# Performance work log

Hardware: AMD Instinct MI355X
Metric: run time of the kernel (lower is better)

The kernel has to match this reference:

```python
import jax, jax.numpy as jnp
import numpy as np

N = 50000   # nodes
E = 600000  # edges
D = 128     # in_channels == heads*hidden_channels
OUT = 64    # out_channels
L = 3       # local_layers
EPS = 1e-5  # BatchNorm eps


def setup_inputs() -> dict:
    key = jax.random.key(0)
    ks = jax.random.split(key, 10)
    s = 0.05
    x = jax.random.normal(ks[0], (N, D), jnp.float32)
    edge_index = jax.random.randint(ks[1], (2, E), 0, N, dtype=jnp.int32)
    Wg = jax.random.normal(ks[2], (L, D, D), jnp.float32) * s  # GCNConv weights
    bg = jnp.zeros((L, D), jnp.float32)                         # GCNConv biases
    Wl = jax.random.normal(ks[3], (L, D, D), jnp.float32) * s  # residual Linear weights
    bl = jax.random.normal(ks[4], (L, D), jnp.float32) * s
    gamma = jnp.ones((L, D), jnp.float32)                       # BN scale
    beta = jnp.zeros((L, D), jnp.float32)                       # BN shift
    Wp = jax.random.normal(ks[5], (D, OUT), jnp.float32) * s   # pred head
    bp = jnp.zeros((OUT,), jnp.float32)
    return {"x": x, "edge_index": edge_index, "Wg": Wg, "bg": bg,
            "Wl": Wl, "bl": bl, "gamma": gamma, "beta": beta,
            "Wp": Wp, "bp": bp}


def reference(x, edge_index, Wg, bg, Wl, bl, gamma, beta, Wp, bp):
    src, dst = edge_index[0], edge_index[1]
    # GCN symmetric normalization with self-loops (PyG gcn_norm):
    # deg computed on target (col) including self-loop.
    deg = jax.ops.segment_sum(jnp.ones((E,), x.dtype), dst, num_segments=N) + 1.0
    dinv = jax.lax.rsqrt(deg)                      # deg^{-1/2}, [N]
    enorm = dinv[src] * dinv[dst]                  # per-edge norm, [E]
    self_norm = (dinv * dinv)[:, None]             # deg^{-1} for self-loop, [N,1]

    h = x
    x_local = jnp.zeros((N, D), x.dtype)
    for i in range(L):
        hg = h @ Wg[i]                             # [N, D] transformed features
        # gather -> weight -> scatter-add (message passing) + self-loop term
        agg = jax.ops.segment_sum(hg[src] * enorm[:, None], dst, num_segments=N)
        conv = agg + hg * self_norm + bg[i]
        # residual linear
        h = conv + h @ Wl[i] + bl[i]
        # BatchNorm1d (training-mode batch statistics, biased var)
        mu = jnp.mean(h, axis=0)
        var = jnp.mean(jnp.square(h - mu), axis=0)
        h = (h - mu) * jax.lax.rsqrt(var + EPS) * gamma[i] + beta[i]
        h = jax.nn.relu(h)
        x_local = x_local + h                      # add_ accumulation
    return x_local @ Wp + bp
```

## Files before the change

### kernel.cpp

```cpp
#include <hip/hip_runtime.h>

#define D 128
#define OUTC 64
#define EC 256

typedef float floatx4 __attribute__((ext_vector_type(4)));
typedef short short8 __attribute__((ext_vector_type(8)));

__device__ inline unsigned short f2bf(float f) {
  unsigned int u = __float_as_uint(f);
  unsigned int r = (u + 0x7FFF + ((u >> 16) & 1)) >> 16;
  return (unsigned short)r;
}
__device__ inline float bf2f(unsigned short u) {
  return __uint_as_float(((unsigned int)u) << 16);
}

__device__ inline int swz(int row, int k) { return row * 128 + (k ^ ((row & 7) << 3)); }

__global__ __launch_bounds__(256) void k_prepx(const float* __restrict__ x, unsigned short* __restrict__ xb, int total4) {
  int stride = gridDim.x * blockDim.x;
  for (int i = blockIdx.x * blockDim.x + threadIdx.x; i < total4; i += stride) {
    float4 v = ((const float4*)x)[i];
    ushort4 o;
    o.x = f2bf(v.x); o.y = f2bf(v.y); o.z = f2bf(v.z); o.w = f2bf(v.w);
    ((ushort4*)xb)[i] = o;
  }
}

__global__ __launch_bounds__(256) void k_prepw(const float* __restrict__ Wg, const float* __restrict__ Wl,
                                               const float* __restrict__ Wp,
                                               unsigned short* __restrict__ Wgt, unsigned short* __restrict__ Wlt,
                                               unsigned short* __restrict__ Wpt) {
  int u = blockIdx.x * 256 + threadIdx.x;
  const int W1 = 3 * D * D;
  if (u < W1) {
    int i = u / (D * D), rem = u % (D * D);
    int k = rem / D, n = rem % D;
    Wgt[i * D * D + n * D + k] = f2bf(Wg[u]);
  } else if (u < 2 * W1) {
    int v = u - W1;
    int i = v / (D * D), rem = v % (D * D);
    int k = rem / D, n = rem % D;
    Wlt[i * D * D + n * D + k] = f2bf(Wl[v]);
  } else if (u < 2 * W1 + D * OUTC) {
    int v = u - 2 * W1;
    int k = v / OUTC, n = v % OUTC;
    Wpt[n * D + k] = f2bf(Wp[v]);
  }
}


__global__ __launch_bounds__(256) void k_bh(const int* __restrict__ dst, int* __restrict__ bh,
                                            int E, int nbuk, int chk) {
  __shared__ int hist[256];
  int t = threadIdx.x, c = blockIdx.x;
  hist[t] = 0;
  __syncthreads();
  int s = c * chk, e = min(E, s + chk);
  for (int j = s + t; j < e; j += 256)
    atomicAdd(&hist[dst[j] >> 8], 1);
  __syncthreads();
  if (t < nbuk) bh[t * EC + c] = hist[t];
}

__device__ inline int block_scan4(int4 v, int t, int* total) {
  int s = v.x + v.y + v.z + v.w;
  int lane = t & 63, w = t >> 6;
  int incl = s;
  #pragma unroll
  for (int off = 1; off < 64; off <<= 1) {
    int nb = __shfl_up(incl, off);
    if (lane >= off) incl += nb;
  }
  __shared__ int wsum[4];
  if (lane == 63) wsum[w] = incl;
  __syncthreads();
  int woff = 0;
  #pragma unroll
  for (int k = 0; k < 3; ++k) if (w > k) woff += wsum[k];
  if (total) *total = wsum[0] + wsum[1] + wsum[2] + wsum[3];
  return woff + incl - s;
}

__global__ __launch_bounds__(256) void k_gscan1(int* __restrict__ arr, int* __restrict__ bsum, int n) {
  int t = threadIdx.x;
  int i0 = blockIdx.x * 1024 + t * 4;
  int4 v = make_int4(0, 0, 0, 0);
  if (i0 + 3 < n) v = *(const int4*)(arr + i0);
  else {
    if (i0 < n) v.x = arr[i0];
    if (i0 + 1 < n) v.y = arr[i0 + 1];
    if (i0 + 2 < n) v.z = arr[i0 + 2];
    if (i0 + 3 < n) v.w = arr[i0 + 3];
  }
  int total;
  int e = block_scan4(v, t, &total);
  if (i0 < n) {
    int4 o;
    o.x = e; o.y = e + v.x; o.z = o.y + v.y; o.w = o.z + v.z;
    if (i0 + 3 < n) *(int4*)(arr + i0) = o;
    else {
      arr[i0] = o.x;
      if (i0 + 1 < n) arr[i0 + 1] = o.y;
      if (i0 + 2 < n) arr[i0 + 2] = o.z;
    }
  }
  if (t == 0) bsum[blockIdx.x] = total;
}

__global__ __launch_bounds__(256) void k_gscan2(int* __restrict__ bsum, int nb) {
  int t = threadIdx.x;
  int i0 = t * 4;
  int4 v = make_int4(0, 0, 0, 0);
  if (i0 + 3 < nb) v = *(const int4*)(bsum + i0);
  else {
    if (i0 < nb) v.x = bsum[i0];
    if (i0 + 1 < nb) v.y = bsum[i0 + 1];
    if (i0 + 2 < nb) v.z = bsum[i0 + 2];
    if (i0 + 3 < nb) v.w = bsum[i0 + 3];
  }
  int e = block_scan4(v, t, nullptr);
  if (i0 < nb) {
    bsum[i0] = e;
    if (i0 + 1 < nb) bsum[i0 + 1] = e + v.x;
    if (i0 + 2 < nb) bsum[i0 + 2] = e + v.x + v.y;
    if (i0 + 3 < nb) bsum[i0 + 3] = e + v.x + v.y + v.z;
  }
}

__global__ __launch_bounds__(256) void k_scatter(const int* __restrict__ src, const int* __restrict__ dst,
                                                 const int* __restrict__ bhs, const int* __restrict__ bsum,
                                                 unsigned int* __restrict__ ebuk, int E, int nbuk, int chk) {
  __shared__ int cur[256];
  int t = threadIdx.x, c = blockIdx.x;
  if (t < nbuk) {
    int idx = t * EC + c;
    cur[t] = bhs[idx] + bsum[idx >> 10];
  }
  __syncthreads();
  int s = c * chk, e = min(E, s + chk);
  for (int j = s + t; j < e; j += 256) {
    int d = dst[j];
    int pos = atomicAdd(&cur[d >> 8], 1);
    ebuk[pos] = (unsigned int)src[j] | ((unsigned int)(d & 255) << 24);
  }
}

__global__ __launch_bounds__(256) void k_csr(const unsigned int* __restrict__ ebuk, const int* __restrict__ bhs,
                                             const int* __restrict__ bsum,
                                             int* __restrict__ rowstart, int* __restrict__ csr,
                                             float* __restrict__ dinv, int E, int N, int nbuk) {
  __shared__ int cnt[256];
  __shared__ int wsum[4];
  int t = threadIdx.x, b = blockIdx.x;
  int si = b * EC;
  int s = bhs[si] + bsum[si >> 10];
  int e;
  if (b + 1 < nbuk) { int ei_ = (b + 1) * EC; e = bhs[ei_] + bsum[ei_ >> 10]; }
  else e = E;
  cnt[t] = 0;
  __syncthreads();
  for (int j = s + t; j < e; j += 256)
    atomicAdd(&cnt[ebuk[j] >> 24], 1);
  __syncthreads();
  int v = cnt[t];
  int lane = t & 63, w = t >> 6;
  int incl = v;
  #pragma unroll
  for (int off = 1; off < 64; off <<= 1) {
    int nb = __shfl_up(incl, off);
    if (lane >= off) incl += nb;
  }
  if (lane == 63) wsum[w] = incl;
  __syncthreads();
  int woff = 0;
  #pragma unroll
  for (int k = 0; k < 3; ++k) if (w > k) woff += wsum[k];
  int rs = s + woff + incl - v;
  int node = (b << 8) + t;
  __syncthreads();
  cnt[t] = rs;
  if (node < N) {
    rowstart[node] = rs;
    dinv[node] = rsqrtf((float)v + 1.0f);
  }
  if (node == 0) rowstart[N] = E;
  __syncthreads();
  for (int j = s + t; j < e; j += 256) {
    unsigned int ed = ebuk[j];
    int pos = atomicAdd(&cnt[ed >> 24], 1);
    csr[pos] = (int)(ed & 0xFFFFFFu);
  }
}

__global__ __launch_bounds__(256) void k_dual(const unsigned short* __restrict__ Ab,
                                              const unsigned short* __restrict__ Wgt,
                                              const unsigned short* __restrict__ Wlt,
                                              const float* __restrict__ bg, const float* __restrict__ bl,
                                              unsigned short* __restrict__ hg, unsigned short* __restrict__ hl, int M) {
  __shared__ unsigned short As[64 * 128];
  __shared__ unsigned short Bs[128 * 128];
  int tid = threadIdx.x;
  int row0 = blockIdx.x * 64;

  {
    int r = tid >> 2;
    int row = row0 + r;
    const unsigned short* src = Ab + (size_t)row * D;
    #pragma unroll
    for (int j = 0; j < 4; ++j) {
      int c = (tid & 3) + j * 4;
      short8 v = {0, 0, 0, 0, 0, 0, 0, 0};
      if (row < M) v = *(const short8*)(src + c * 8);
      *(short8*)&As[swz(r, c * 8)] = v;
    }
  }
  #pragma unroll
  for (int j = 0; j < 8; ++j) {
    int idx = tid + j * 256;
    int nr = idx >> 4, c = idx & 15;
    *(short8*)&Bs[swz(nr, c * 8)] = *(const short8*)(Wgt + nr * D + c * 8);
  }
  __syncthreads();

  int lane = tid & 63, w = tid >> 6;
  int lrow = lane & 15, lk = (lane >> 4) * 8;

  short8 af[4][4];
  #pragma unroll
  for (int m = 0; m < 4; ++m) {
    int ar = lrow + m * 16;
    #pragma unroll
    for (int kk = 0; kk < 4; ++kk)
      af[m][kk] = *(const short8*)&As[swz(ar, lk + kk * 32)];
  }

  {
    short8 bfg[2][4];
    #pragma unroll
    for (int n = 0; n < 2; ++n) {
      int br = w * 32 + n * 16 + lrow;
      #pragma unroll
      for (int kk = 0; kk < 4; ++kk)
        bfg[n][kk] = *(const short8*)&Bs[swz(br, lk + kk * 32)];
    }
    floatx4 acc[4][2];
    #pragma unroll
    for (int m = 0; m < 4; ++m)
      #pragma unroll
      for (int n = 0; n < 2; ++n)
        acc[m][n] = (floatx4)0.0f;
    #pragma unroll
    for (int kk = 0; kk < 4; ++kk)
      #pragma unroll
      for (int m = 0; m < 4; ++m)
        #pragma unroll
        for (int n = 0; n < 2; ++n)
          acc[m][n] = __builtin_amdgcn_mfma_f32_16x16x32_bf16(af[m][kk], bfg[n][kk], acc[m][n], 0, 0, 0);
    #pragma unroll
    for (int m = 0; m < 4; ++m)
      #pragma unroll
      for (int n = 0; n < 2; ++n) {
        int col = w * 32 + n * 16 + lrow;
        #pragma unroll
        for (int reg = 0; reg < 4; ++reg) {
          int row = row0 + m * 16 + (lane >> 4) * 4 + reg;
          if (row < M) hg[(size_t)row * D + col] = f2bf(acc[m][n][reg]);
        }
      }
  }
  __syncthreads();
  #pragma unroll
  for (int j = 0; j < 8; ++j) {
    int idx = tid + j * 256;
    int nr = idx >> 4, c = idx & 15;
    *(short8*)&Bs[swz(nr, c * 8)] = *(const short8*)(Wlt + nr * D + c * 8);
  }
  __syncthreads();
  {
    short8 bfl[2][4];
    #pragma unroll
    for (int n = 0; n < 2; ++n) {
      int br = w * 32 + n * 16 + lrow;
      #pragma unroll
      for (int kk = 0; kk < 4; ++kk)
        bfl[n][kk] = *(const short8*)&Bs[swz(br, lk + kk * 32)];
    }
    floatx4 acc[4][2];
    #pragma unroll
    for (int m = 0; m < 4; ++m)
      #pragma unroll
      for (int n = 0; n < 2; ++n)
        acc[m][n] = (floatx4)0.0f;
    #pragma unroll
    for (int kk = 0; kk < 4; ++kk)
      #pragma unroll
      for (int m = 0; m < 4; ++m)
        #pragma unroll
        for (int n = 0; n < 2; ++n)
          acc[m][n] = __builtin_amdgcn_mfma_f32_16x16x32_bf16(af[m][kk], bfl[n][kk], acc[m][n], 0, 0, 0);
    #pragma unroll
    for (int m = 0; m < 4; ++m)
      #pragma unroll
      for (int n = 0; n < 2; ++n) {
        int col = w * 32 + n * 16 + lrow;
        float bias = bg[col] + bl[col];
        #pragma unroll
        for (int reg = 0; reg < 4; ++reg) {
          int row = row0 + m * 16 + (lane >> 4) * 4 + reg;
          if (row < M) hl[(size_t)row * D + col] = f2bf(acc[m][n][reg] + bias);
        }
      }
  }
}

__global__ __launch_bounds__(256) void k_agg(const unsigned short* __restrict__ hg, unsigned short* __restrict__ pre,
                                             const int* __restrict__ rowstart, const int* __restrict__ csr,
                                             const float* __restrict__ dinv,
                                             float* __restrict__ partial, int n) {
  int t = threadIdx.x, b = blockIdx.x;
  int w = t >> 6, lane = t & 63;
  const unsigned int* base = (const unsigned int*)hg;
  unsigned int* prew = (unsigned int*)pre;
  float st_s0 = 0.f, st_s1 = 0.f, st_q0 = 0.f, st_q1 = 0.f;
  int c = lane * 2;
  int node0 = b * 16 + w * 4;
  #pragma unroll 1
  for (int k = 0; k < 4; ++k) {
    int node = node0 + k;
    if (node >= n) break;
    int s = rowstart[node], e = rowstart[node + 1];
    float dn = dinv[node];
    unsigned int ps = base[(size_t)node * 64 + lane];
    unsigned int oldw = prew[(size_t)node * 64 + lane];
    float a0 = 0.f, a1 = 0.f, b0 = 0.f, b1 = 0.f;
    float c0 = 0.f, c1 = 0.f, d0 = 0.f, d1 = 0.f;
    int j = s;
    for (; j + 4 <= e; j += 4) {
      int sn0 = csr[j], sn1 = csr[j + 1], sn2 = csr[j + 2], sn3 = csr[j + 3];
      float w0 = dinv[sn0], w1 = dinv[sn1], w2 = dinv[sn2], w3 = dinv[sn3];
      unsigned int p0 = base[(size_t)sn0 * 64 + lane];
      unsigned int p1 = base[(size_t)sn1 * 64 + lane];
      unsigned int p2 = base[(size_t)sn2 * 64 + lane];
      unsigned int p3 = base[(size_t)sn3 * 64 + lane];
      a0 += w0 * __uint_as_float(p0 << 16); a1 += w0 * __uint_as_float(p0 & 0xFFFF0000u);
      b0 += w1 * __uint_as_float(p1 << 16); b1 += w1 * __uint_as_float(p1 & 0xFFFF0000u);
      c0 += w2 * __uint_as_float(p2 << 16); c1 += w2 * __uint_as_float(p2 & 0xFFFF0000u);
      d0 += w3 * __uint_as_float(p3 << 16); d1 += w3 * __uint_as_float(p3 & 0xFFFF0000u);
    }
    for (; j < e; ++j) {
      int sn = csr[j];
      float wv = dinv[sn];
      unsigned int p = base[(size_t)sn * 64 + lane];
      a0 += wv * __uint_as_float(p << 16);
      a1 += wv * __uint_as_float(p & 0xFFFF0000u);
    }
    float acc0 = (a0 + b0) + (c0 + d0);
    float acc1 = (a1 + b1) + (c1 + d1);
    float sf = dn * dn;
    float h0 = __uint_as_float(ps << 16);
    float h1 = __uint_as_float(ps & 0xFFFF0000u);
    float old0 = __uint_as_float(oldw << 16);
    float old1 = __uint_as_float(oldw & 0xFFFF0000u);
    float p0 = dn * acc0 + h0 * sf + old0;
    float p1 = dn * acc1 + h1 * sf + old1;
    prew[(size_t)node * 64 + lane] = (unsigned int)f2bf(p0) | ((unsigned int)f2bf(p1) << 16);
    st_s0 += p0; st_s1 += p1;
    st_q0 += p0 * p0; st_q1 += p1 * p1;
  }
  __shared__ float sm[4][128], sq[4][128];
  sm[w][c] = st_s0; sm[w][c + 1] = st_s1;
  sq[w][c] = st_q0; sq[w][c + 1] = st_q1;
  __syncthreads();
  if (t < 128) {
    float s = (sm[0][t] + sm[1][t]) + (sm[2][t] + sm[3][t]);
    float q = (sq[0][t] + sq[1][t]) + (sq[2][t] + sq[3][t]);
    partial[(size_t)b * 256 + t] = s;
    partial[(size_t)b * 256 + 128 + t] = q;
  }
}

__global__ __launch_bounds__(256) void k_fina(const float* __restrict__ partial, float* __restrict__ p2, int nab) {
  int t = threadIdx.x, b = blockIdx.x;
  float s = 0.f;
  for (int i = b; i < nab; i += 64)
    s += partial[(size_t)i * 256 + t];
  p2[(size_t)b * 256 + t] = s;
}

__global__ __launch_bounds__(256) void k_finb(const float* __restrict__ p2,
                                              const float* __restrict__ gamma, const float* __restrict__ beta,
                                              float* __restrict__ ab, float invN) {
  int t = threadIdx.x;
  float s = 0.f;
  #pragma unroll
  for (int b = 0; b < 64; ++b)
    s += p2[(size_t)b * 256 + t];
  __shared__ float red[256];
  red[t] = s;
  __syncthreads();
  if (t < 128) {
    float mean = red[t] * invN;
    float var = red[128 + t] * invN - mean * mean;
    float inv = rsqrtf(var + 1e-5f);
    float g = gamma[t];
    ab[t] = g * inv;
    ab[128 + t] = beta[t] - mean * inv * g;
  }
}

template<bool FIRST>
__global__ __launch_bounds__(256) void k_fused(const unsigned short* __restrict__ pre, const float* __restrict__ ab,
                                               const unsigned short* __restrict__ Wpt, const float* __restrict__ bp,
                                               const unsigned short* __restrict__ Wgt,
                                               const unsigned short* __restrict__ Wlt,
                                               const float* __restrict__ bgn, const float* __restrict__ bln,
                                               float* __restrict__ out, unsigned short* __restrict__ hg,
                                               unsigned short* __restrict__ hl, int M) {
  __shared__ unsigned short As[64 * 128];
  __shared__ unsigned short Bs[128 * 128];
  int tid = threadIdx.x;
  int row0 = blockIdx.x * 64;

  {
    int r = tid >> 2, qq = tid & 3;
    int row = row0 + r;
    bool valid = row < M;
    const unsigned short* Pp = pre + (size_t)row * D;
    #pragma unroll
    for (int ch = 0; ch < 4; ++ch) {
      int k0 = qq * 32 + ch * 8;
      short8 pv = {0, 0, 0, 0, 0, 0, 0, 0};
      if (valid) pv = *(const short8*)(Pp + k0);
      float4 a0 = *(const float4*)(ab + k0),        a1 = *(const float4*)(ab + k0 + 4);
      float4 b0 = *(const float4*)(ab + 128 + k0),  b1 = *(const float4*)(ab + 128 + k0 + 4);
      float av[8] = {a0.x, a0.y, a0.z, a0.w, a1.x, a1.y, a1.z, a1.w};
      float bv[8] = {b0.x, b0.y, b0.z, b0.w, b1.x, b1.y, b1.z, b1.w};
      unsigned short hv[8];
      #pragma unroll
      for (int jj = 0; jj < 8; ++jj) {
        float f = bf2f((unsigned short)pv[jj]);
        hv[jj] = f2bf(fmaxf(f * av[jj] + bv[jj], 0.f));
      }
      *(short8*)&As[swz(r, k0)] = *(const short8*)hv;
    }
  }
  #pragma unroll
  for (int j = 0; j < 4; ++j) {
    int idx = tid + j * 256;
    int nr = idx >> 4, c = idx & 15;
    *(short8*)&Bs[swz(nr, c * 8)] = *(const short8*)(Wpt + nr * D + c * 8);
  }
  __syncthreads();

  int lane = tid & 63, w = tid >> 6;
  int lrow = lane & 15, lk = (lane >> 4) * 8;

  short8 af[4][4];
  #pragma unroll
  for (int m = 0; m < 4; ++m) {
    int ar = lrow + m * 16;
    #pragma unroll
    for (int kk = 0; kk < 4; ++kk)
      af[m][kk] = *(const short8*)&As[swz(ar, lk + kk * 32)];
  }

  {
    short8 bfr[4];
    int br = w * 16 + lrow;
    #pragma unroll
    for (int kk = 0; kk < 4; ++kk)
      bfr[kk] = *(const short8*)&Bs[swz(br, lk + kk * 32)];
    floatx4 acc[4];
    #pragma unroll
    for (int m = 0; m < 4; ++m) acc[m] = (floatx4)0.0f;
    #pragma unroll
    for (int kk = 0; kk < 4; ++kk)
      #pragma unroll
      for (int m = 0; m < 4; ++m)
        acc[m] = __builtin_amdgcn_mfma_f32_16x16x32_bf16(af[m][kk], bfr[kk], acc[m], 0, 0, 0);
    int col = w * 16 + lrow;
    float bpv = FIRST ? bp[col] : 0.f;
    #pragma unroll
    for (int m = 0; m < 4; ++m)
      #pragma unroll
      for (int reg = 0; reg < 4; ++reg) {
        int row = row0 + m * 16 + (lane >> 4) * 4 + reg;
        if (row < M) {
          float* op = &out[(size_t)row * OUTC + col];
          float v = acc[m][reg] + bpv;
          if (!FIRST) v += *op;
          *op = v;
        }
      }
  }
  __syncthreads();
  #pragma unroll
  for (int j = 0; j < 8; ++j) {
    int idx = tid + j * 256;
    int nr = idx >> 4, c = idx & 15;
    *(short8*)&Bs[swz(nr, c * 8)] = *(const short8*)(Wgt + nr * D + c * 8);
  }
  __syncthreads();
  {
    short8 bfg[2][4];
    #pragma unroll
    for (int n = 0; n < 2; ++n) {
      int br = w * 32 + n * 16 + lrow;
      #pragma unroll
      for (int kk = 0; kk < 4; ++kk)
        bfg[n][kk] = *(const short8*)&Bs[swz(br, lk + kk * 32)];
    }
    floatx4 acc[4][2];
    #pragma unroll
    for (int m = 0; m < 4; ++m)
      #pragma unroll
      for (int n = 0; n < 2; ++n)
        acc[m][n] = (floatx4)0.0f;
    #pragma unroll
    for (int kk = 0; kk < 4; ++kk)
      #pragma unroll
      for (int m = 0; m < 4; ++m)
        #pragma unroll
        for (int n = 0; n < 2; ++n)
          acc[m][n] = __builtin_amdgcn_mfma_f32_16x16x32_bf16(af[m][kk], bfg[n][kk], acc[m][n], 0, 0, 0);
    #pragma unroll
    for (int m = 0; m < 4; ++m)
      #pragma unroll
      for (int n = 0; n < 2; ++n) {
        int col = w * 32 + n * 16 + lrow;
        #pragma unroll
        for (int reg = 0; reg < 4; ++reg) {
          int row = row0 + m * 16 + (lane >> 4) * 4 + reg;
          if (row < M) hg[(size_t)row * D + col] = f2bf(acc[m][n][reg]);
        }
      }
  }
  __syncthreads();
  #pragma unroll
  for (int j = 0; j < 8; ++j) {
    int idx = tid + j * 256;
    int nr = idx >> 4, c = idx & 15;
    *(short8*)&Bs[swz(nr, c * 8)] = *(const short8*)(Wlt + nr * D + c * 8);
  }
  __syncthreads();
  {
    short8 bfl[2][4];
    #pragma unroll
    for (int n = 0; n < 2; ++n) {
      int br = w * 32 + n * 16 + lrow;
      #pragma unroll
      for (int kk = 0; kk < 4; ++kk)
        bfl[n][kk] = *(const short8*)&Bs[swz(br, lk + kk * 32)];
    }
    floatx4 acc[4][2];
    #pragma unroll
    for (int m = 0; m < 4; ++m)
      #pragma unroll
      for (int n = 0; n < 2; ++n)
        acc[m][n] = (floatx4)0.0f;
    #pragma unroll
    for (int kk = 0; kk < 4; ++kk)
      #pragma unroll
      for (int m = 0; m < 4; ++m)
        #pragma unroll
        for (int n = 0; n < 2; ++n)
          acc[m][n] = __builtin_amdgcn_mfma_f32_16x16x32_bf16(af[m][kk], bfl[n][kk], acc[m][n], 0, 0, 0);
    #pragma unroll
    for (int m = 0; m < 4; ++m)
      #pragma unroll
      for (int n = 0; n < 2; ++n) {
        int col = w * 32 + n * 16 + lrow;
        float bias = bgn[col] + bln[col];
        #pragma unroll
        for (int reg = 0; reg < 4; ++reg) {
          int row = row0 + m * 16 + (lane >> 4) * 4 + reg;
          if (row < M) hl[(size_t)row * D + col] = f2bf(acc[m][n][reg] + bias);
        }
      }
  }
}

__global__ __launch_bounds__(256) void k_out(const unsigned short* __restrict__ pre, const float* __restrict__ ab,
                                             const unsigned short* __restrict__ Wpt,
                                             float* __restrict__ out, int M) {
  __shared__ unsigned short As[64 * 128];
  __shared__ unsigned short Bs[OUTC * 128];
  int tid = threadIdx.x;
  int row0 = blockIdx.x * 64;

  {
    int r = tid >> 2, qq = tid & 3;
    int row = row0 + r;
    bool valid = row < M;
    const unsigned short* Pp = pre + (size_t)row * D;
    #pragma unroll
    for (int ch = 0; ch < 4; ++ch) {
      int k0 = qq * 32 + ch * 8;
      short8 pv = {0, 0, 0, 0, 0, 0, 0, 0};
      if (valid) pv = *(const short8*)(Pp + k0);
      float4 a0 = *(const float4*)(ab + k0),        a1 = *(const float4*)(ab + k0 + 4);
      float4 b0 = *(const float4*)(ab + 128 + k0),  b1 = *(const float4*)(ab + 128 + k0 + 4);
      float av[8] = {a0.x, a0.y, a0.z, a0.w, a1.x, a1.y, a1.z, a1.w};
      float bv[8] = {b0.x, b0.y, b0.z, b0.w, b1.x, b1.y, b1.z, b1.w};
      unsigned short hv[8];
      #pragma unroll
      for (int jj = 0; jj < 8; ++jj) {
        float f = bf2f((unsigned short)pv[jj]);
        hv[jj] = f2bf(fmaxf(f * av[jj] + bv[jj], 0.f));
      }
      *(short8*)&As[swz(r, k0)] = *(const short8*)hv;
    }
  }
  #pragma unroll
  for (int j = 0; j < 4; ++j) {
    int idx = tid + j * 256;
    int nr = idx >> 4, c = idx & 15;
    *(short8*)&Bs[swz(nr, c * 8)] = *(const short8*)(Wpt + nr * D + c * 8);
  }
  __syncthreads();

  int lane = tid & 63, w = tid >> 6;
  int lrow = lane & 15, lk = (lane >> 4) * 8;

  short8 af[4][4];
  #pragma unroll
  for (int m = 0; m < 4; ++m) {
    int ar = lrow + m * 16;
    #pragma unroll
    for (int kk = 0; kk < 4; ++kk)
      af[m][kk] = *(const short8*)&As[swz(ar, lk + kk * 32)];
  }
  short8 bfr[4];
  {
    int br = w * 16 + lrow;
    #pragma unroll
    for (int kk = 0; kk < 4; ++kk)
      bfr[kk] = *(const short8*)&Bs[swz(br, lk + kk * 32)];
  }
  floatx4 acc[4];
  #pragma unroll
  for (int m = 0; m < 4; ++m) acc[m] = (floatx4)0.0f;
  #pragma unroll
  for (int kk = 0; kk < 4; ++kk)
    #pragma unroll
    for (int m = 0; m < 4; ++m)
      acc[m] = __builtin_amdgcn_mfma_f32_16x16x32_bf16(af[m][kk], bfr[kk], acc[m], 0, 0, 0);

  int col = w * 16 + lrow;
  #pragma unroll
  for (int m = 0; m < 4; ++m)
    #pragma unroll
    for (int reg = 0; reg < 4; ++reg) {
      int row = row0 + m * 16 + (lane >> 4) * 4 + reg;
      if (row < M) {
        float* op = &out[(size_t)row * OUTC + col];
        *op = *op + acc[m][reg];
      }
    }
}

extern "C" void kernel_launch(void* const* d_in, const int* in_sizes, int n_in,
                              void* d_out, int out_size, void* d_ws, size_t ws_size,
                              hipStream_t stream) {
  const float* x     = (const float*)d_in[0];
  const int*   ei    = (const int*)d_in[1];
  const float* Wg    = (const float*)d_in[2];
  const float* bg    = (const float*)d_in[3];
  const float* Wl    = (const float*)d_in[4];
  const float* bl    = (const float*)d_in[5];
  const float* gamma = (const float*)d_in[6];
  const float* beta  = (const float*)d_in[7];
  const float* Wp    = (const float*)d_in[8];
  const float* bp    = (const float*)d_in[9];
  float* out = (float*)d_out;

  int N = in_sizes[0] / D;
  int E = in_sizes[1] / 2;
  const int* srcp = ei;
  const int* dstp = ei + E;

  char* wsb = (char*)d_ws;
  size_t off = 0;
  auto alloc = [&](size_t bytes) {
    off = (off + 255) & ~(size_t)255;
    void* p = wsb + off;
    off += bytes;
    return p;
  };
  int nab = (N + 15) / 16;
  float* dinv     = (float*)alloc((size_t)N * 4);
  int*   rowstart = (int*)alloc((size_t)(N + 1) * 4);
  int*   csr      = (int*)alloc((size_t)E * 4);
  int*   bh       = (int*)alloc((size_t)256 * EC * 4);
  unsigned int* ebuk = (unsigned int*)alloc((size_t)E * 4);
  int*   bsum     = (int*)alloc(1024 * 4);
  float* partial  = (float*)alloc((size_t)nab * 256 * 4);
  float* p2       = (float*)alloc((size_t)64 * 256 * 4);
  float* ab       = (float*)alloc(3 * 256 * 4);
  unsigned short* xb  = (unsigned short*)alloc((size_t)N * D * 2);
  unsigned short* hg  = (unsigned short*)alloc((size_t)N * D * 2);
  unsigned short* hl  = (unsigned short*)alloc((size_t)N * D * 2);
  unsigned short* Wgt = (unsigned short*)alloc(3 * D * D * 2);
  unsigned short* Wlt = (unsigned short*)alloc(3 * D * D * 2);
  unsigned short* Wpt = (unsigned short*)alloc(D * OUTC * 2);
  (void)ws_size; (void)n_in; (void)out_size;

  k_prepx<<<1024, 256, 0, stream>>>(x, xb, N * D / 4);
  int wtotal = 2 * 3 * D * D + D * OUTC;
  k_prepw<<<(wtotal + 255) / 256, 256, 0, stream>>>(Wg, Wl, Wp, Wgt, Wlt, Wpt);

  int nbuk = (N + 255) >> 8;
  int chk  = (E + EC - 1) / EC;
  k_bh<<<EC, 256, 0, stream>>>(dstp, bh, E, nbuk, chk);
  int sn  = nbuk * EC;
  int snb = (sn + 1023) >> 10;
  k_gscan1<<<snb, 256, 0, stream>>>(bh, bsum, sn);
  k_gscan2<<<1, 256, 0, stream>>>(bsum, snb);
  k_scatter<<<EC, 256, 0, stream>>>(srcp, dstp, bh, bsum, ebuk, E, nbuk, chk);
  k_csr<<<nbuk, 256, 0, stream>>>(ebuk, bh, bsum, rowstart, csr, dinv, E, N, nbuk);

  int mt = (N + 63) / 64;
  float invN = 1.0f / (float)N;

  k_dual<<<mt, 256, 0, stream>>>(xb, Wgt, Wlt, bg, bl, hg, hl, N);

  for (int i = 0; i < 3; ++i) {
    k_agg<<<nab, 256, 0, stream>>>(hg, hl, rowstart, csr, dinv, partial, N);
    k_fina<<<64, 256, 0, stream>>>(partial, p2, nab);
    k_finb<<<1, 256, 0, stream>>>(p2, gamma + (size_t)i * D, beta + (size_t)i * D, ab + i * 256, invN);
    if (i == 0)
      k_fused<true><<<mt, 256, 0, stream>>>(hl, ab + i * 256, Wpt, bp,
                                            Wgt + (size_t)(i + 1) * D * D, Wlt + (size_t)(i + 1) * D * D,
                                            bg + (size_t)(i + 1) * D, bl + (size_t)(i + 1) * D,
                                            out, hg, hl, N);
    else if (i == 1)
      k_fused<false><<<mt, 256, 0, stream>>>(hl, ab + i * 256, Wpt, bp,
                                             Wgt + (size_t)(i + 1) * D * D, Wlt + (size_t)(i + 1) * D * D,
                                             bg + (size_t)(i + 1) * D, bl + (size_t)(i + 1) * D,
                                             out, hg, hl, N);
    else
      k_out<<<mt, 256, 0, stream>>>(hl, ab + i * 256, Wpt, out, N);
  }
}
```

Baseline: 290.3 us.

## Prescale GEMM output by dinv so aggregation skips per-edge dinv gathers

The GEMM kernels now multiply each transformed row by its node's dinv before storing it as bf16. The aggregation kernel can then sum neighbour rows directly and apply the target node's dinv once, which drops one random dinv gather and multiply per edge. The edge loop is also widened to eight independent accumulators, with a clamped, predicated tail in place of the scalar remainder loop, to keep more loads in flight. Rounding to bf16 now happens after scaling by dinv, which slightly changes numerics.

```diff
diff --git a/kernel.cpp b/kernel.cpp
--- a/kernel.cpp
+++ b/kernel.cpp
@@ -198,12 +198,15 @@
                                               const unsigned short* __restrict__ Wgt,
                                               const unsigned short* __restrict__ Wlt,
                                               const float* __restrict__ bg, const float* __restrict__ bl,
+                                              const float* __restrict__ dinv,
                                               unsigned short* __restrict__ hg, unsigned short* __restrict__ hl, int M) {
   __shared__ unsigned short As[64 * 128];
   __shared__ unsigned short Bs[128 * 128];
+  __shared__ float sdinv[64];
   int tid = threadIdx.x;
   int row0 = blockIdx.x * 64;
 
+  if (tid < 64) sdinv[tid] = (row0 + tid < M) ? dinv[row0 + tid] : 0.f;
   {
     int r = tid >> 2;
     int row = row0 + r;
@@ -265,8 +268,9 @@
         int col = w * 32 + n * 16 + lrow;
         #pragma unroll
         for (int reg = 0; reg < 4; ++reg) {
-          int row = row0 + m * 16 + (lane >> 4) * 4 + reg;
-          if (row < M) hg[(size_t)row * D + col] = f2bf(acc[m][n][reg]);
+          int lr = m * 16 + (lane >> 4) * 4 + reg;
+          int row = row0 + lr;
+          if (row < M) hg[(size_t)row * D + col] = f2bf(sdinv[lr] * acc[m][n][reg]);
         }
       }
   }
@@ -315,13 +319,13 @@
   }
 }
 
-__global__ __launch_bounds__(256) void k_agg(const unsigned short* __restrict__ hg, unsigned short* __restrict__ pre,
+__global__ __launch_bounds__(256) void k_agg(const unsigned short* __restrict__ hg2, unsigned short* __restrict__ pre,
                                              const int* __restrict__ rowstart, const int* __restrict__ csr,
                                              const float* __restrict__ dinv,
                                              float* __restrict__ partial, int n) {
   int t = threadIdx.x, b = blockIdx.x;
   int w = t >> 6, lane = t & 63;
-  const unsigned int* base = (const unsigned int*)hg;
+  const unsigned int* base = (const unsigned int*)hg2;
   unsigned int* prew = (unsigned int*)pre;
   float st_s0 = 0.f, st_s1 = 0.f, st_q0 = 0.f, st_q1 = 0.f;
   int c = lane * 2;
@@ -334,40 +338,61 @@
     float dn = dinv[node];
     unsigned int ps = base[(size_t)node * 64 + lane];
     unsigned int oldw = prew[(size_t)node * 64 + lane];
-    float a0 = 0.f, a1 = 0.f, b0 = 0.f, b1 = 0.f;
-    float c0 = 0.f, c1 = 0.f, d0 = 0.f, d1 = 0.f;
+    float A0 = 0.f, A1 = 0.f, B0 = 0.f, B1 = 0.f, C0 = 0.f, C1 = 0.f, D0 = 0.f, D1 = 0.f;
+    float E0 = 0.f, E1 = 0.f, F0 = 0.f, F1 = 0.f, G0 = 0.f, G1 = 0.f, H0 = 0.f, H1 = 0.f;
     int j = s;
-    for (; j + 4 <= e; j += 4) {
-      int sn0 = csr[j], sn1 = csr[j + 1], sn2 = csr[j + 2], sn3 = csr[j + 3];
-      float w0 = dinv[sn0], w1 = dinv[sn1], w2 = dinv[sn2], w3 = dinv[sn3];
-      unsigned int p0 = base[(size_t)sn0 * 64 + lane];
-      unsigned int p1 = base[(size_t)sn1 * 64 + lane];
-      unsigned int p2 = base[(size_t)sn2 * 64 + lane];
-      unsigned int p3 = base[(size_t)sn3 * 64 + lane];
-      a0 += w0 * __uint_as_float(p0 << 16); a1 += w0 * __uint_as_float(p0 & 0xFFFF0000u);
-      b0 += w1 * __uint_as_float(p1 << 16); b1 += w1 * __uint_as_float(p1 & 0xFFFF0000u);
-      c0 += w2 * __uint_as_float(p2 << 16); c1 += w2 * __uint_as_float(p2 & 0xFFFF0000u);
-      d0 += w3 * __uint_as_float(p3 << 16); d1 += w3 * __uint_as_float(p3 & 0xFFFF0000u);
-    }
-    for (; j < e; ++j) {
-      int sn = csr[j];
-      float wv = dinv[sn];
-      unsigned int p = base[(size_t)sn * 64 + lane];
-      a0 += wv * __uint_as_float(p << 16);
-      a1 += wv * __uint_as_float(p & 0xFFFF0000u);
-    }
-    float acc0 = (a0 + b0) + (c0 + d0);
-    float acc1 = (a1 + b1) + (c1 + d1);
-    float sf = dn * dn;
+    for (; j + 8 <= e; j += 8) {
+      int i0 = csr[j],     i1 = csr[j + 1], i2 = csr[j + 2], i3 = csr[j + 3];
+      int i4 = csr[j + 4], i5 = csr[j + 5], i6 = csr[j + 6], i7 = csr[j + 7];
+      unsigned int p0 = base[(size_t)i0 * 64 + lane];
+      unsigned int p1 = base[(size_t)i1 * 64 + lane];
+      unsigned int p2 = base[(size_t)i2 * 64 + lane];
+      unsigned int p3 = base[(size_t)i3 * 64 + lane];
+      unsigned int p4 = base[(size_t)i4 * 64 + lane];
+      unsigned int p5 = base[(size_t)i5 * 64 + lane];
+      unsigned int p6 = base[(size_t)i6 * 64 + lane];
+      unsigned int p7 = base[(size_t)i7 * 64 + lane];
+      A0 += __uint_as_float(p0 << 16); A1 += __uint_as_float(p0 & 0xFFFF0000u);
+      B0 += __uint_as_float(p1 << 16); B1 += __uint_as_float(p1 & 0xFFFF0000u);
+      C0 += __uint_as_float(p2 << 16); C1 += __uint_as_float(p2 & 0xFFFF0000u);
+      D0 += __uint_as_float(p3 << 16); D1 += __uint_as_float(p3 & 0xFFFF0000u);
+      E0 += __uint_as_float(p4 << 16); E1 += __uint_as_float(p4 & 0xFFFF0000u);
+      F0 += __uint_as_float(p5 << 16); F1 += __uint_as_float(p5 & 0xFFFF0000u);
+      G0 += __uint_as_float(p6 << 16); G1 += __uint_as_float(p6 & 0xFFFF0000u);
+      H0 += __uint_as_float(p7 << 16); H1 += __uint_as_float(p7 & 0xFFFF0000u);
+    }
+    if (j < e) {
+      int last = e - 1;
+      int i0 = csr[j];
+      int i1 = csr[min(j + 1, last)], i2 = csr[min(j + 2, last)], i3 = csr[min(j + 3, last)];
+      int i4 = csr[min(j + 4, last)], i5 = csr[min(j + 5, last)], i6 = csr[min(j + 6, last)];
+      unsigned int p0 = base[(size_t)i0 * 64 + lane];
+      unsigned int p1 = base[(size_t)i1 * 64 + lane];
+      unsigned int p2 = base[(size_t)i2 * 64 + lane];
+      unsigned int p3 = base[(size_t)i3 * 64 + lane];
+      unsigned int p4 = base[(size_t)i4 * 64 + lane];
+      unsigned int p5 = base[(size_t)i5 * 64 + lane];
+      unsigned int p6 = base[(size_t)i6 * 64 + lane];
+      int r = e - j;
+      A0 += __uint_as_float(p0 << 16);                     A1 += __uint_as_float(p0 & 0xFFFF0000u);
+      if (r > 1) { B0 += __uint_as_float(p1 << 16);        B1 += __uint_as_float(p1 & 0xFFFF0000u); }
+      if (r > 2) { C0 += __uint_as_float(p2 << 16);        C1 += __uint_as_float(p2 & 0xFFFF0000u); }
+      if (r > 3) { D0 += __uint_as_float(p3 << 16);        D1 += __uint_as_float(p3 & 0xFFFF0000u); }
+      if (r > 4) { E0 += __uint_as_float(p4 << 16);        E1 += __uint_as_float(p4 & 0xFFFF0000u); }
+      if (r > 5) { F0 += __uint_as_float(p5 << 16);        F1 += __uint_as_float(p5 & 0xFFFF0000u); }
+      if (r > 6) { G0 += __uint_as_float(p6 << 16);        G1 += __uint_as_float(p6 & 0xFFFF0000u); }
+    }
+    float acc0 = ((A0 + B0) + (C0 + D0)) + ((E0 + F0) + (G0 + H0));
+    float acc1 = ((A1 + B1) + (C1 + D1)) + ((E1 + F1) + (G1 + H1));
     float h0 = __uint_as_float(ps << 16);
     float h1 = __uint_as_float(ps & 0xFFFF0000u);
     float old0 = __uint_as_float(oldw << 16);
     float old1 = __uint_as_float(oldw & 0xFFFF0000u);
-    float p0 = dn * acc0 + h0 * sf + old0;
-    float p1 = dn * acc1 + h1 * sf + old1;
-    prew[(size_t)node * 64 + lane] = (unsigned int)f2bf(p0) | ((unsigned int)f2bf(p1) << 16);
-    st_s0 += p0; st_s1 += p1;
-    st_q0 += p0 * p0; st_q1 += p1 * p1;
+    float p0v = dn * (acc0 + h0) + old0;
+    float p1v = dn * (acc1 + h1) + old1;
+    prew[(size_t)node * 64 + lane] = (unsigned int)f2bf(p0v) | ((unsigned int)f2bf(p1v) << 16);
+    st_s0 += p0v; st_s1 += p1v;
+    st_q0 += p0v * p0v; st_q1 += p1v * p1v;
   }
   __shared__ float sm[4][128], sq[4][128];
   sm[w][c] = st_s0; sm[w][c + 1] = st_s1;
@@ -416,13 +441,16 @@
                                                const unsigned short* __restrict__ Wgt,
                                                const unsigned short* __restrict__ Wlt,
                                                const float* __restrict__ bgn, const float* __restrict__ bln,
+                                               const float* __restrict__ dinv,
                                                float* __restrict__ out, unsigned short* __restrict__ hg,
                                                unsigned short* __restrict__ hl, int M) {
   __shared__ unsigned short As[64 * 128];
   __shared__ unsigned short Bs[128 * 128];
+  __shared__ float sdinv[64];
   int tid = threadIdx.x;
   int row0 = blockIdx.x * 64;
 
+  if (tid < 64) sdinv[tid] = (row0 + tid < M) ? dinv[row0 + tid] : 0.f;
   {
     int r = tid >> 2, qq = tid & 3;
     int row = row0 + r;
@@ -532,8 +560,9 @@
         int col = w * 32 + n * 16 + lrow;
         #pragma unroll
         for (int reg = 0; reg < 4; ++reg) {
-          int row = row0 + m * 16 + (lane >> 4) * 4 + reg;
-          if (row < M) hg[(size_t)row * D + col] = f2bf(acc[m][n][reg]);
+          int lr = m * 16 + (lane >> 4) * 4 + reg;
+          int row = row0 + lr;
+          if (row < M) hg[(size_t)row * D + col] = f2bf(sdinv[lr] * acc[m][n][reg]);
         }
       }
   }
@@ -724,7 +753,7 @@
   int mt = (N + 63) / 64;
   float invN = 1.0f / (float)N;
 
-  k_dual<<<mt, 256, 0, stream>>>(xb, Wgt, Wlt, bg, bl, hg, hl, N);
+  k_dual<<<mt, 256, 0, stream>>>(xb, Wgt, Wlt, bg, bl, dinv, hg, hl, N);
 
   for (int i = 0; i < 3; ++i) {
     k_agg<<<nab, 256, 0, stream>>>(hg, hl, rowstart, csr, dinv, partial, N);
@@ -734,12 +763,12 @@
       k_fused<true><<<mt, 256, 0, stream>>>(hl, ab + i * 256, Wpt, bp,
                                             Wgt + (size_t)(i + 1) * D * D, Wlt + (size_t)(i + 1) * D * D,
                                             bg + (size_t)(i + 1) * D, bl + (size_t)(i + 1) * D,
-                                            out, hg, hl, N);
+                                            dinv, out, hg, hl, N);
     else if (i == 1)
       k_fused<false><<<mt, 256, 0, stream>>>(hl, ab + i * 256, Wpt, bp,
                                              Wgt + (size_t)(i + 1) * D * D, Wlt + (size_t)(i + 1) * D * D,
                                              bg + (size_t)(i + 1) * D, bl + (size_t)(i + 1) * D,
-                                             out, hg, hl, N);
+                                             dinv, out, hg, hl, N);
     else
       k_out<<<mt, 256, 0, stream>>>(hl, ab + i * 256, Wpt, out, N);
   }
```

Result: faster. 268.3 us (-7.6%).
